# Performance work log

Hardware: AMD Instinct MI355X
Metric: run time of the kernel (lower is better)

## Reference

```python
import jax, jax.numpy as jnp
import numpy as np

EMBED_DIM = 1024
NUM_HEADS = 16
HEAD_DIM = EMBED_DIM // NUM_HEADS


def setup_inputs() -> dict:
    key = jax.random.key(0)
    ks = jax.random.split(key, 10)
    B, S, D = 4, 2048, EMBED_DIM
    s = 1.0 / np.sqrt(D)
    return {
        "x": jax.random.normal(ks[0], (B, S, D), dtype=jnp.float32),
        "Wq": jax.random.normal(ks[1], (D, D), dtype=jnp.float32) * s,
        "bq": jnp.zeros((D,), dtype=jnp.float32),
        "Wk": jax.random.normal(ks[2], (D, D), dtype=jnp.float32) * s,
        "bk": jnp.zeros((D,), dtype=jnp.float32),
        "Wv": jax.random.normal(ks[3], (D, D), dtype=jnp.float32) * s,
        "bv": jnp.zeros((D,), dtype=jnp.float32),
        "Wo": jax.random.normal(ks[4], (D, D), dtype=jnp.float32) * s,
        "bo": jnp.zeros((D,), dtype=jnp.float32),
        "ln_w": jnp.ones((D,), dtype=jnp.float32),
        "ln_b": jnp.zeros((D,), dtype=jnp.float32),
    }


def _layernorm(x, w, b, eps=1e-5):
    mu = jnp.mean(x, axis=-1, keepdims=True)
    var = jnp.mean(jnp.square(x - mu), axis=-1, keepdims=True)
    return (x - mu) * jax.lax.rsqrt(var + eps) * w + b


def reference(x, Wq, bq, Wk, bk, Wv, bv, Wo, bo, ln_w, ln_b):
    B, S, D = x.shape
    H, hd = NUM_HEADS, HEAD_DIM
    # projections (torch Linear: x @ W.T + b)
    q = (x @ Wq.T + bq).reshape(B, S, H, hd).transpose(0, 2, 1, 3)  # [B,H,S,hd]
    k = (x @ Wk.T + bk).reshape(B, S, H, hd).transpose(0, 2, 1, 3)
    v = (x @ Wv.T + bv).reshape(B, S, H, hd).transpose(0, 2, 1, 3)
    scores = jnp.einsum("bhqd,bhkd->bhqk", q, k) / np.sqrt(hd)
    attn = jax.nn.softmax(scores, axis=-1)
    out = jnp.einsum("bhqk,bhkd->bhqd", attn, v)
    out = out.transpose(0, 2, 1, 3).reshape(B, S, D)
    out = out @ Wo.T + bo
    return _layernorm(out, ln_w, ln_b)
```

## Files before the change

kernel.cpp:

```cpp
#include <hip/hip_runtime.h>
#include <hip/hip_bf16.h>
#include <math.h>

typedef unsigned short u16;
typedef unsigned int   u32;
typedef short bf16x8 __attribute__((ext_vector_type(8)));
typedef float f32x4  __attribute__((ext_vector_type(4)));
typedef float f32x16 __attribute__((ext_vector_type(16)));
typedef u32   u32x4  __attribute__((ext_vector_type(4)));
typedef u32   u32x2  __attribute__((ext_vector_type(2)));

#define B_   4
#define S_   2048
#define D_   1024
#define H_   16
#define HD_  64
#define M_   (B_*S_)

static __device__ __forceinline__ u16 f2bf(float f) {
  __hip_bfloat16 h = __float2bfloat16(f);
  return *reinterpret_cast<u16*>(&h);
}
static __device__ __forceinline__ u32 pack_bf(float lo, float hi) {
  return (u32)f2bf(lo) | ((u32)f2bf(hi) << 16);
}
static __device__ __forceinline__ u32 pack_bf_trunc(float lo, float hi) {
  return __builtin_amdgcn_perm(__float_as_uint(hi), __float_as_uint(lo), 0x07060302u);
}
static __device__ __forceinline__ f32x16 zero16() {
  f32x16 z;
#pragma unroll
  for (int i = 0; i < 16; ++i) z[i] = 0.f;
  return z;
}

typedef __attribute__((address_space(1))) const u32* gas_t;
typedef __attribute__((address_space(3))) u32* las_t;
static __device__ __forceinline__ void g2l16(const void* g, void* l) {
  __builtin_amdgcn_global_load_lds((gas_t)g, (las_t)l, 16, 0, 0);
}

__global__ __launch_bounds__(256) void cast_all(const float* __restrict__ x,
                                                const float* __restrict__ Wq,
                                                const float* __restrict__ Wk,
                                                const float* __restrict__ Wv,
                                                const float* __restrict__ Wo,
                                                u16* __restrict__ xb,
                                                u16* __restrict__ Wqb,
                                                u16* __restrict__ Wkb,
                                                u16* __restrict__ Wvb,
                                                u16* __restrict__ Wob) {
  int bid = blockIdx.x;
  const float* src;
  u16* dst;
  int off;
  if (bid < 8192) {
    src = x; dst = xb; off = bid;
  } else {
    int t = bid - 8192;
    int w = t >> 10;
    off   = t & 1023;
    src = w == 0 ? Wq : w == 1 ? Wk : w == 2 ? Wv : Wo;
    dst = w == 0 ? Wqb : w == 1 ? Wkb : w == 2 ? Wvb : Wob;
  }
  int i = (off * 256 + threadIdx.x) * 4;
  float4 v = *reinterpret_cast<const float4*>(src + i);
  uint2 o;
  o.x = pack_bf(v.x, v.y);
  o.y = pack_bf(v.z, v.w);
  *reinterpret_cast<uint2*>(dst + i) = o;
}

__global__ __launch_bounds__(256) void gemm_qkv(const u16* __restrict__ A,
                                                const u16* __restrict__ Wq,
                                                const u16* __restrict__ Wk,
                                                const u16* __restrict__ Wv,
                                                const float* __restrict__ bq,
                                                const float* __restrict__ bk,
                                                const float* __restrict__ bv,
                                                u16* __restrict__ Qo,
                                                u16* __restrict__ Ko,
                                                u16* __restrict__ Vo) {
  const int tid  = threadIdx.x;
  const int lane = tid & 63;
  const int wave = tid >> 6;
  const int m16  = lane & 15;
  const int quad = lane >> 4;
  const int wm   = wave & 1;
  const int wn   = wave >> 1;

  const int bid  = blockIdx.x;
  const int xcd  = bid & 7;
  const int j    = bid >> 3;
  const int which = j >> 6;
  const int jj   = j & 63;
  const int m0   = (xcd * 8 + (jj >> 3)) * 128;
  const int n0   = (jj & 7) * 128;

  const u16* W = which == 0 ? Wq : which == 1 ? Wk : Wv;
  const float* bias = which == 0 ? bq : which == 1 ? bk : bv;

  __shared__ __align__(16) u16 As[128 * 32];
  __shared__ __align__(16) u16 Bs[128 * 32];

  f32x4 acc[4][4];
#pragma unroll
  for (int i = 0; i < 4; ++i)
#pragma unroll
    for (int j2 = 0; j2 < 4; ++j2) acc[i][j2] = (f32x4){0.f, 0.f, 0.f, 0.f};

  const int eA = (wave << 6) + lane;
  const int eB = 256 + (wave << 6) + lane;
  const int r0_ = eA >> 2, c0_ = (eA & 3) * 8;
  const int r1_ = eB >> 2, c1_ = (eB & 3) * 8;
  const u16* pa0 = A + (size_t)(m0 + r0_) * 1024 + c0_;
  const u16* pa1 = A + (size_t)(m0 + r1_) * 1024 + c1_;
  const u16* pw0 = W + (size_t)(n0 + r0_) * 1024 + c0_;
  const u16* pw1 = W + (size_t)(n0 + r1_) * 1024 + c1_;
  u16* lA0 = &As[((wave << 6)) * 8];
  u16* lA1 = &As[((wave << 6) + 256) * 8];
  u16* lB0 = &Bs[((wave << 6)) * 8];
  u16* lB1 = &Bs[((wave << 6) + 256) * 8];

  for (int t = 0; t < 32; ++t) {
    g2l16(pa0, lA0);
    g2l16(pw0, lB0);
    g2l16(pa1, lA1);
    g2l16(pw1, lB1);
    pa0 += 32; pa1 += 32; pw0 += 32; pw1 += 32;
    __syncthreads();

    bf16x8 af[4], bfr[4];
#pragma unroll
    for (int mt = 0; mt < 4; ++mt)
      af[mt] = *reinterpret_cast<const bf16x8*>(&As[(wm * 64 + mt * 16 + m16) * 32 + quad * 8]);
#pragma unroll
    for (int nt = 0; nt < 4; ++nt)
      bfr[nt] = *reinterpret_cast<const bf16x8*>(&Bs[(wn * 64 + nt * 16 + m16) * 32 + quad * 8]);

#pragma unroll
    for (int mt = 0; mt < 4; ++mt)
#pragma unroll
      for (int nt = 0; nt < 4; ++nt)
        acc[mt][nt] = __builtin_amdgcn_mfma_f32_16x16x32_bf16(af[mt], bfr[nt], acc[mt][nt], 0, 0, 0);
    __syncthreads();
  }

  const float scale = which == 0 ? 0.125f * 1.44269504f : 1.0f;
  u16* ob = which == 0 ? Qo : which == 1 ? Ko : Vo;
#pragma unroll
  for (int mt = 0; mt < 4; ++mt) {
#pragma unroll
    for (int nt = 0; nt < 4; ++nt) {
      int col = n0 + wn * 64 + nt * 16 + m16;
      float bi = bias[col];
      int row0 = m0 + wm * 64 + mt * 16 + quad * 4;
      int b = row0 >> 11, s = row0 & 2047;
      int h = col >> 6,  d = col & 63;
      float v[4];
#pragma unroll
      for (int r = 0; r < 4; ++r) v[r] = (acc[mt][nt][r] + bi) * scale;
      if (which < 2) {
#pragma unroll
        for (int r = 0; r < 4; ++r)
          ob[(size_t)((b * H_ + h) * S_ + s + r) * HD_ + d] = f2bf(v[r]);
      } else {
        uint2 w;
        w.x = pack_bf(v[0], v[1]);
        w.y = pack_bf(v[2], v[3]);
        *reinterpret_cast<uint2*>(&ob[(size_t)((b * H_ + h) * HD_ + d) * S_ + s]) = w;
      }
    }
  }
}

__global__ __launch_bounds__(256) void gemm_bt(const u16* __restrict__ A,
                                               const u16* __restrict__ W,
                                               const float* __restrict__ bias,
                                               float* __restrict__ out) {
  const int tid  = threadIdx.x;
  const int lane = tid & 63;
  const int wave = tid >> 6;
  const int m16  = lane & 15;
  const int quad = lane >> 4;
  const int wm   = wave & 1;
  const int wn   = wave >> 1;

  const int bid = blockIdx.x;
  const int xcd = bid & 7;
  const int j   = bid >> 3;
  const int m0  = (xcd * 8 + (j >> 3)) * 128;
  const int n0  = (j & 7) * 128;

  __shared__ __align__(16) u16 As[128 * 32];
  __shared__ __align__(16) u16 Bs[128 * 32];

  f32x4 acc[4][4];
#pragma unroll
  for (int i = 0; i < 4; ++i)
#pragma unroll
    for (int j2 = 0; j2 < 4; ++j2) acc[i][j2] = (f32x4){0.f, 0.f, 0.f, 0.f};

  const int eA = (wave << 6) + lane;
  const int eB = 256 + (wave << 6) + lane;
  const int r0_ = eA >> 2, c0_ = (eA & 3) * 8;
  const int r1_ = eB >> 2, c1_ = (eB & 3) * 8;
  const u16* pa0 = A + (size_t)(m0 + r0_) * 1024 + c0_;
  const u16* pa1 = A + (size_t)(m0 + r1_) * 1024 + c1_;
  const u16* pw0 = W + (size_t)(n0 + r0_) * 1024 + c0_;
  const u16* pw1 = W + (size_t)(n0 + r1_) * 1024 + c1_;
  u16* lA0 = &As[((wave << 6)) * 8];
  u16* lA1 = &As[((wave << 6) + 256) * 8];
  u16* lB0 = &Bs[((wave << 6)) * 8];
  u16* lB1 = &Bs[((wave << 6) + 256) * 8];

  for (int t = 0; t < 32; ++t) {
    g2l16(pa0, lA0);
    g2l16(pw0, lB0);
    g2l16(pa1, lA1);
    g2l16(pw1, lB1);
    pa0 += 32; pa1 += 32; pw0 += 32; pw1 += 32;
    __syncthreads();

    bf16x8 af[4], bfr[4];
#pragma unroll
    for (int mt = 0; mt < 4; ++mt)
      af[mt] = *reinterpret_cast<const bf16x8*>(&As[(wm * 64 + mt * 16 + m16) * 32 + quad * 8]);
#pragma unroll
    for (int nt = 0; nt < 4; ++nt)
      bfr[nt] = *reinterpret_cast<const bf16x8*>(&Bs[(wn * 64 + nt * 16 + m16) * 32 + quad * 8]);

#pragma unroll
    for (int mt = 0; mt < 4; ++mt)
#pragma unroll
      for (int nt = 0; nt < 4; ++nt)
        acc[mt][nt] = __builtin_amdgcn_mfma_f32_16x16x32_bf16(af[mt], bfr[nt], acc[mt][nt], 0, 0, 0);
    __syncthreads();
  }

#pragma unroll
  for (int mt = 0; mt < 4; ++mt) {
#pragma unroll
    for (int nt = 0; nt < 4; ++nt) {
      int col = n0 + wn * 64 + nt * 16 + m16;
      float bi = bias[col];
#pragma unroll
      for (int r = 0; r < 4; ++r) {
        int row = m0 + wm * 64 + mt * 16 + quad * 4 + r;
        out[(size_t)row * 1024 + col] = acc[mt][nt][r] + bi;
      }
    }
  }
}

__global__ __launch_bounds__(256, 4) void attn_kernel(const u16* __restrict__ Q,
                                                      const u16* __restrict__ K,
                                                      const u16* __restrict__ Vt,
                                                      u16* __restrict__ out) {
  const int tid  = threadIdx.x;
  const int lane = tid & 63;
  const int wave = tid >> 6;
  const int r32  = lane & 31;
  const int h32  = lane >> 5;

  const int bid = blockIdx.x;
  const int swz = (bid & 7) * 128 + (bid >> 3);
  const int bh  = swz >> 4;
  const int q0  = (swz & 15) * 128 + wave * 32;

  __shared__ __align__(16) u16 Ks[2][64 * 72];
  __shared__ __align__(16) u16 Vs[2][64 * 72];

  const u16* kbase = K  + (size_t)bh * S_ * HD_;
  const u16* vbase = Vt + (size_t)bh * HD_ * S_;
  const int e  = tid;
  const int e2 = tid + 256;
  const int row_a = e >> 3,  c8_a = (e & 7) * 8;
  const int row_b = e2 >> 3, c8_b = (e2 & 7) * 8;

  bf16x8 qf[4];
  {
    const u16* qbase = Q + (size_t)(bh * S_ + q0 + r32) * HD_ + h32 * 8;
#pragma unroll
    for (int dc = 0; dc < 4; ++dc)
      qf[dc] = *reinterpret_cast<const bf16x8*>(qbase + dc * 16);
  }

  f32x16 acc[2];
#pragma unroll
  for (int dt = 0; dt < 2; ++dt) acc[dt] = zero16();
  float lsum = 0.f;

  const u16* pkp0 = kbase + (size_t)row_a * HD_ + c8_a;
  const u16* pkp1 = kbase + (size_t)row_b * HD_ + c8_b;
  const u16* pvp0 = vbase + (size_t)row_a * S_ + c8_a;
  const u16* pvp1 = vbase + (size_t)row_b * S_ + c8_b;

  uint4 kr0 = *reinterpret_cast<const uint4*>(pkp0);
  uint4 kr1 = *reinterpret_cast<const uint4*>(pkp1);
  uint4 vr0 = *reinterpret_cast<const uint4*>(pvp0);
  uint4 vr1 = *reinterpret_cast<const uint4*>(pvp1);

  const int NT = S_ / 64;
  for (int kt = 0; kt < NT; ++kt) {
    u16* ks = Ks[kt & 1];
    u16* vs = Vs[kt & 1];
    *reinterpret_cast<uint4*>(&ks[row_a * 72 + c8_a]) = kr0;
    *reinterpret_cast<uint4*>(&ks[row_b * 72 + c8_b]) = kr1;
    *reinterpret_cast<uint4*>(&vs[row_a * 72 + c8_a]) = vr0;
    *reinterpret_cast<uint4*>(&vs[row_b * 72 + c8_b]) = vr1;
    __syncthreads();

    pkp0 += 64 * HD_; pkp1 += 64 * HD_; pvp0 += 64; pvp1 += 64;
    kr0 = *reinterpret_cast<const uint4*>(pkp0);
    kr1 = *reinterpret_cast<const uint4*>(pkp1);
    vr0 = *reinterpret_cast<const uint4*>(pvp0);
    vr1 = *reinterpret_cast<const uint4*>(pvp1);

    f32x16 sc[2];
    __builtin_amdgcn_s_setprio(1);
#pragma unroll
    for (int nt = 0; nt < 2; ++nt) {
      sc[nt] = zero16();
#pragma unroll
      for (int dc = 0; dc < 4; ++dc) {
        bf16x8 kf = *reinterpret_cast<const bf16x8*>(&ks[(nt * 32 + r32) * 72 + dc * 16 + h32 * 8]);
        sc[nt] = __builtin_amdgcn_mfma_f32_32x32x16_bf16(kf, qf[dc], sc[nt], 0, 0, 0);
      }
    }
    __builtin_amdgcn_s_setprio(0);

    u32 pk[2][8];
    float ps0 = 0.f, ps1 = 0.f;
#pragma unroll
    for (int nt = 0; nt < 2; ++nt)
#pragma unroll
      for (int i = 0; i < 8; ++i) {
        float p0 = __builtin_amdgcn_exp2f(sc[nt][2 * i]);
        float p1 = __builtin_amdgcn_exp2f(sc[nt][2 * i + 1]);
        ps0 += p0;
        ps1 += p1;
        pk[nt][i] = pack_bf_trunc(p0, p1);
      }
    lsum += ps0 + ps1;

    __builtin_amdgcn_s_setprio(1);
#pragma unroll
    for (int nt = 0; nt < 2; ++nt) {
#pragma unroll
      for (int kc2 = 0; kc2 < 2; ++kc2) {
        u32x2 r0 = __builtin_amdgcn_permlane32_swap(pk[nt][4 * kc2 + 0], pk[nt][4 * kc2 + 2], false, false);
        u32x2 r1 = __builtin_amdgcn_permlane32_swap(pk[nt][4 * kc2 + 1], pk[nt][4 * kc2 + 3], false, false);
        u32x4 bw;
        bw[0] = r0[0];
        bw[1] = r1[0];
        bw[2] = r0[1];
        bw[3] = r1[1];
        bf16x8 pfrag = *reinterpret_cast<bf16x8*>(&bw);
        const int kc = nt * 2 + kc2;
#pragma unroll
        for (int dt = 0; dt < 2; ++dt) {
          bf16x8 vf = *reinterpret_cast<const bf16x8*>(&vs[(dt * 32 + r32) * 72 + kc * 16 + h32 * 8]);
          acc[dt] = __builtin_amdgcn_mfma_f32_32x32x16_bf16(vf, pfrag, acc[dt], 0, 0, 0);
        }
      }
    }
    __builtin_amdgcn_s_setprio(0);
  }

  const int b = bh >> 4, hh = bh & 15;
  float lt  = lsum + __shfl_xor(lsum, 32);
  float inv = 1.f / lt;
  int srow = q0 + r32;
  u16* orow = out + (size_t)(b * S_ + srow) * D_ + hh * HD_;
#pragma unroll
  for (int dt = 0; dt < 2; ++dt) {
#pragma unroll
    for (int g = 0; g < 4; ++g) {
      u32x2 w;
      w[0] = pack_bf(acc[dt][4 * g + 0] * inv, acc[dt][4 * g + 1] * inv);
      w[1] = pack_bf(acc[dt][4 * g + 2] * inv, acc[dt][4 * g + 3] * inv);
      __builtin_nontemporal_store(w, reinterpret_cast<u32x2*>(orow + dt * 32 + 8 * g + 4 * h32));
    }
  }
}

__global__ __launch_bounds__(256) void ln_kernel(const float* __restrict__ X,
                                                 const float* __restrict__ w,
                                                 const float* __restrict__ b,
                                                 float* __restrict__ out) {
  const int row = blockIdx.x;
  const int tid = threadIdx.x;
  const float* x = X + (size_t)row * 1024;
  float vals[4];
  float s = 0.f, s2 = 0.f;
#pragma unroll
  for (int i = 0; i < 4; ++i) {
    float v = x[tid + i * 256];
    vals[i] = v;
    s += v;
    s2 += v * v;
  }
#pragma unroll
  for (int off = 32; off; off >>= 1) {
    s  += __shfl_xor(s, off);
    s2 += __shfl_xor(s2, off);
  }
  __shared__ float a1[4], a2[4];
  if ((tid & 63) == 0) { a1[tid >> 6] = s; a2[tid >> 6] = s2; }
  __syncthreads();
  s  = a1[0] + a1[1] + a1[2] + a1[3];
  s2 = a2[0] + a2[1] + a2[2] + a2[3];
  float mu  = s * (1.f / 1024.f);
  float var = s2 * (1.f / 1024.f) - mu * mu;
  float inv = rsqrtf(var + 1e-5f);
#pragma unroll
  for (int i = 0; i < 4; ++i) {
    int c = tid + i * 256;
    out[(size_t)row * 1024 + c] = (vals[i] - mu) * inv * w[c] + b[c];
  }
}

extern "C" void kernel_launch(void* const* d_in, const int* in_sizes, int n_in,
                              void* d_out, int out_size, void* d_ws, size_t ws_size,
                              hipStream_t stream) {
  const float* x   = (const float*)d_in[0];
  const float* Wq  = (const float*)d_in[1];
  const float* bq  = (const float*)d_in[2];
  const float* Wk  = (const float*)d_in[3];
  const float* bk  = (const float*)d_in[4];
  const float* Wv  = (const float*)d_in[5];
  const float* bv  = (const float*)d_in[6];
  const float* Wo  = (const float*)d_in[7];
  const float* bo  = (const float*)d_in[8];
  const float* lnw = (const float*)d_in[9];
  const float* lnb = (const float*)d_in[10];

  const size_t MB = 1024ull * 1024ull;
  char* ws = (char*)d_ws;
  u16* xb  = (u16*)(ws + 0);
  u16* Qb  = (u16*)(ws + 16 * MB);
  u16* Kb  = (u16*)(ws + 32 * MB);
  u16* Vtb = (u16*)(ws + 48 * MB);
  u16* Wqb = (u16*)(ws + 64 * MB);
  u16* Wkb = (u16*)(ws + 66 * MB);
  u16* Wvb = (u16*)(ws + 68 * MB);
  u16* Wob = (u16*)(ws + 70 * MB);
  float* Of = (float*)(ws + 16 * MB);

  cast_all<<<8192 + 4096, 256, 0, stream>>>(x, Wq, Wk, Wv, Wo, xb, Wqb, Wkb, Wvb, Wob);

  gemm_qkv<<<(M_ / 128) * 3 * (D_ / 128), 256, 0, stream>>>(
      xb, Wqb, Wkb, Wvb, bq, bk, bv, Qb, Kb, Vtb);

  attn_kernel<<<(S_ / 128) * B_ * H_, 256, 0, stream>>>(Qb, Kb, Vtb, xb);

  gemm_bt<<<(M_ / 128) * (D_ / 128), 256, 0, stream>>>(xb, Wob, bo, Of);

  ln_kernel<<<M_, 256, 0, stream>>>(Of, lnw, lnb, (float*)d_out);
}
```

Measured before the change: 290.2 us.

## Double-buffer LDS in both GEMMs and simplify attention grid indexing

Both the QKV projection and output projection GEMMs now use two LDS buffers, so the global-to-LDS load for the next K-slice is issued while MFMAs run on the current slice. The aim is to hide memory latency behind compute. The attention kernel drops its XCD-aware block swizzle in favour of a 2D grid, and its nontemporal output stores become plain stores. These changes double LDS use per GEMM block and may hurt L2 locality across XCDs in attention.

```diff
diff --git a/kernel.cpp b/kernel.cpp
--- a/kernel.cpp
+++ b/kernel.cpp
@@ -100,8 +100,8 @@
   const u16* W = which == 0 ? Wq : which == 1 ? Wk : Wv;
   const float* bias = which == 0 ? bq : which == 1 ? bk : bv;
 
-  __shared__ __align__(16) u16 As[128 * 32];
-  __shared__ __align__(16) u16 Bs[128 * 32];
+  __shared__ __align__(16) u16 As[2][128 * 32];
+  __shared__ __align__(16) u16 Bs[2][128 * 32];
 
   f32x4 acc[4][4];
 #pragma unroll
@@ -117,34 +117,49 @@
   const u16* pa1 = A + (size_t)(m0 + r1_) * 1024 + c1_;
   const u16* pw0 = W + (size_t)(n0 + r0_) * 1024 + c0_;
   const u16* pw1 = W + (size_t)(n0 + r1_) * 1024 + c1_;
-  u16* lA0 = &As[((wave << 6)) * 8];
-  u16* lA1 = &As[((wave << 6) + 256) * 8];
-  u16* lB0 = &Bs[((wave << 6)) * 8];
-  u16* lB1 = &Bs[((wave << 6) + 256) * 8];
-
-  for (int t = 0; t < 32; ++t) {
-    g2l16(pa0, lA0);
-    g2l16(pw0, lB0);
-    g2l16(pa1, lA1);
-    g2l16(pw1, lB1);
-    pa0 += 32; pa1 += 32; pw0 += 32; pw1 += 32;
+  const int lds0 = (wave << 6) * 8;
+  const int lds1 = ((wave << 6) + 256) * 8;
+
+#define QKV_STAGE(buf)                                                       \
+  {                                                                          \
+    g2l16(pa0, &As[buf][lds0]);                                              \
+    g2l16(pw0, &Bs[buf][lds0]);                                              \
+    g2l16(pa1, &As[buf][lds1]);                                              \
+    g2l16(pw1, &Bs[buf][lds1]);                                              \
+    pa0 += 32; pa1 += 32; pw0 += 32; pw1 += 32;                              \
+  }
+
+#define QKV_COMPUTE(buf)                                                     \
+  {                                                                          \
+    bf16x8 af[4], bfr[4];                                                    \
+    _Pragma("unroll")                                                        \
+    for (int mt = 0; mt < 4; ++mt)                                           \
+      af[mt] = *reinterpret_cast<const bf16x8*>(                             \
+          &As[buf][(wm * 64 + mt * 16 + m16) * 32 + quad * 8]);              \
+    _Pragma("unroll")                                                        \
+    for (int nt = 0; nt < 4; ++nt)                                           \
+      bfr[nt] = *reinterpret_cast<const bf16x8*>(                            \
+          &Bs[buf][(wn * 64 + nt * 16 + m16) * 32 + quad * 8]);              \
+    _Pragma("unroll")                                                        \
+    for (int mt = 0; mt < 4; ++mt)                                           \
+      _Pragma("unroll")                                                      \
+      for (int nt = 0; nt < 4; ++nt)                                         \
+        acc[mt][nt] = __builtin_amdgcn_mfma_f32_16x16x32_bf16(               \
+            af[mt], bfr[nt], acc[mt][nt], 0, 0, 0);                          \
+  }
+
+  QKV_STAGE(0);
+  __syncthreads();
+  for (int t = 0; t < 32; t += 2) {
+    QKV_STAGE(1);
+    QKV_COMPUTE(0);
     __syncthreads();
-
-    bf16x8 af[4], bfr[4];
-#pragma unroll
-    for (int mt = 0; mt < 4; ++mt)
-      af[mt] = *reinterpret_cast<const bf16x8*>(&As[(wm * 64 + mt * 16 + m16) * 32 + quad * 8]);
-#pragma unroll
-    for (int nt = 0; nt < 4; ++nt)
-      bfr[nt] = *reinterpret_cast<const bf16x8*>(&Bs[(wn * 64 + nt * 16 + m16) * 32 + quad * 8]);
-
-#pragma unroll
-    for (int mt = 0; mt < 4; ++mt)
-#pragma unroll
-      for (int nt = 0; nt < 4; ++nt)
-        acc[mt][nt] = __builtin_amdgcn_mfma_f32_16x16x32_bf16(af[mt], bfr[nt], acc[mt][nt], 0, 0, 0);
+    if (t + 2 < 32) QKV_STAGE(0);
+    QKV_COMPUTE(1);
     __syncthreads();
   }
+#undef QKV_STAGE
+#undef QKV_COMPUTE
 
   const float scale = which == 0 ? 0.125f * 1.44269504f : 1.0f;
   u16* ob = which == 0 ? Qo : which == 1 ? Ko : Vo;
@@ -192,8 +207,8 @@
   const int m0  = (xcd * 8 + (j >> 3)) * 128;
   const int n0  = (j & 7) * 128;
 
-  __shared__ __align__(16) u16 As[128 * 32];
-  __shared__ __align__(16) u16 Bs[128 * 32];
+  __shared__ __align__(16) u16 As[2][128 * 32];
+  __shared__ __align__(16) u16 Bs[2][128 * 32];
 
   f32x4 acc[4][4];
 #pragma unroll
@@ -209,34 +224,49 @@
   const u16* pa1 = A + (size_t)(m0 + r1_) * 1024 + c1_;
   const u16* pw0 = W + (size_t)(n0 + r0_) * 1024 + c0_;
   const u16* pw1 = W + (size_t)(n0 + r1_) * 1024 + c1_;
-  u16* lA0 = &As[((wave << 6)) * 8];
-  u16* lA1 = &As[((wave << 6) + 256) * 8];
-  u16* lB0 = &Bs[((wave << 6)) * 8];
-  u16* lB1 = &Bs[((wave << 6) + 256) * 8];
-
-  for (int t = 0; t < 32; ++t) {
-    g2l16(pa0, lA0);
-    g2l16(pw0, lB0);
-    g2l16(pa1, lA1);
-    g2l16(pw1, lB1);
-    pa0 += 32; pa1 += 32; pw0 += 32; pw1 += 32;
+  const int lds0 = (wave << 6) * 8;
+  const int lds1 = ((wave << 6) + 256) * 8;
+
+#define BT_STAGE(buf)                                                        \
+  {                                                                          \
+    g2l16(pa0, &As[buf][lds0]);                                              \
+    g2l16(pw0, &Bs[buf][lds0]);                                              \
+    g2l16(pa1, &As[buf][lds1]);                                              \
+    g2l16(pw1, &Bs[buf][lds1]);                                              \
+    pa0 += 32; pa1 += 32; pw0 += 32; pw1 += 32;                              \
+  }
+
+#define BT_COMPUTE(buf)                                                      \
+  {                                                                          \
+    bf16x8 af[4], bfr[4];                                                    \
+    _Pragma("unroll")                                                        \
+    for (int mt = 0; mt < 4; ++mt)                                           \
+      af[mt] = *reinterpret_cast<const bf16x8*>(                             \
+          &As[buf][(wm * 64 + mt * 16 + m16) * 32 + quad * 8]);              \
+    _Pragma("unroll")                                                        \
+    for (int nt = 0; nt < 4; ++nt)                                           \
+      bfr[nt] = *reinterpret_cast<const bf16x8*>(                            \
+          &Bs[buf][(wn * 64 + nt * 16 + m16) * 32 + quad * 8]);              \
+    _Pragma("unroll")                                                        \
+    for (int mt = 0; mt < 4; ++mt)                                           \
+      _Pragma("unroll")                                                      \
+      for (int nt = 0; nt < 4; ++nt)                                         \
+        acc[mt][nt] = __builtin_amdgcn_mfma_f32_16x16x32_bf16(               \
+            af[mt], bfr[nt], acc[mt][nt], 0, 0, 0);                          \
+  }
+
+  BT_STAGE(0);
+  __syncthreads();
+  for (int t = 0; t < 32; t += 2) {
+    BT_STAGE(1);
+    BT_COMPUTE(0);
     __syncthreads();
-
-    bf16x8 af[4], bfr[4];
-#pragma unroll
-    for (int mt = 0; mt < 4; ++mt)
-      af[mt] = *reinterpret_cast<const bf16x8*>(&As[(wm * 64 + mt * 16 + m16) * 32 + quad * 8]);
-#pragma unroll
-    for (int nt = 0; nt < 4; ++nt)
-      bfr[nt] = *reinterpret_cast<const bf16x8*>(&Bs[(wn * 64 + nt * 16 + m16) * 32 + quad * 8]);
-
-#pragma unroll
-    for (int mt = 0; mt < 4; ++mt)
-#pragma unroll
-      for (int nt = 0; nt < 4; ++nt)
-        acc[mt][nt] = __builtin_amdgcn_mfma_f32_16x16x32_bf16(af[mt], bfr[nt], acc[mt][nt], 0, 0, 0);
+    if (t + 2 < 32) BT_STAGE(0);
+    BT_COMPUTE(1);
     __syncthreads();
   }
+#undef BT_STAGE
+#undef BT_COMPUTE
 
 #pragma unroll
   for (int mt = 0; mt < 4; ++mt) {
@@ -262,11 +292,8 @@
   const int wave = tid >> 6;
   const int r32  = lane & 31;
   const int h32  = lane >> 5;
-
-  const int bid = blockIdx.x;
-  const int swz = (bid & 7) * 128 + (bid >> 3);
-  const int bh  = swz >> 4;
-  const int q0  = (swz & 15) * 128 + wave * 32;
+  const int bh   = blockIdx.y;
+  const int q0   = blockIdx.x * 128 + wave * 32;
 
   __shared__ __align__(16) u16 Ks[2][64 * 72];
   __shared__ __align__(16) u16 Vs[2][64 * 72];
@@ -377,10 +404,10 @@
   for (int dt = 0; dt < 2; ++dt) {
 #pragma unroll
     for (int g = 0; g < 4; ++g) {
-      u32x2 w;
-      w[0] = pack_bf(acc[dt][4 * g + 0] * inv, acc[dt][4 * g + 1] * inv);
-      w[1] = pack_bf(acc[dt][4 * g + 2] * inv, acc[dt][4 * g + 3] * inv);
-      __builtin_nontemporal_store(w, reinterpret_cast<u32x2*>(orow + dt * 32 + 8 * g + 4 * h32));
+      uint2 w;
+      w.x = pack_bf(acc[dt][4 * g + 0] * inv, acc[dt][4 * g + 1] * inv);
+      w.y = pack_bf(acc[dt][4 * g + 2] * inv, acc[dt][4 * g + 3] * inv);
+      *reinterpret_cast<uint2*>(orow + dt * 32 + 8 * g + 4 * h32) = w;
     }
   }
 }
@@ -453,7 +480,7 @@
   gemm_qkv<<<(M_ / 128) * 3 * (D_ / 128), 256, 0, stream>>>(
       xb, Wqb, Wkb, Wvb, bq, bk, bv, Qb, Kb, Vtb);
 
-  attn_kernel<<<(S_ / 128) * B_ * H_, 256, 0, stream>>>(Qb, Kb, Vtb, xb);
+  attn_kernel<<<dim3(S_ / 128, B_ * H_), 256, 0, stream>>>(Qb, Kb, Vtb, xb);
 
   gemm_bt<<<(M_ / 128) * (D_ / 128), 256, 0, stream>>>(xb, Wob, bo, Of);
 
```

New measurement: 311.5 us. 7.4% more time.
